# Optimization experiments

Hardware: AMD Instinct MI355X
Metric: run time of the kernel (lower is better)

The kernel has to match this reference:

```python
import jax, jax.numpy as jnp
import numpy as np

B, L, HID, NH = 8, 512, 768, 12
D = HID // NH
T_HOP, T_EDGE = 32, 64


def setup_inputs() -> dict:
    key = jax.random.key(0)
    ks = jax.random.split(key, 18)
    f = lambda k, s, sc=1.0: jax.random.normal(k, s, dtype=jnp.float32) * sc
    return {
        "x": f(ks[0], (B, L, HID)),
        "query_hop_emb": f(ks[1], (T_HOP, HID), 0.05),
        "query_edge_emb": f(ks[2], (T_EDGE, HID), 0.05),
        "key_hop_emb": f(ks[3], (T_HOP, HID), 0.05),
        "key_edge_emb": f(ks[4], (T_EDGE, HID), 0.05),
        "value_hop_emb": f(ks[5], (T_HOP, HID), 0.05),
        "value_edge_emb": f(ks[6], (T_EDGE, HID), 0.05),
        "hop": jax.random.randint(ks[7], (B, L, L), 0, T_HOP, dtype=jnp.int32),
        "edge_matrix": jax.random.randint(ks[8], (B, L, L), 0, T_EDGE, dtype=jnp.int32),
        "Wq": f(ks[9], (HID, HID), 0.02), "bq": f(ks[10], (HID,), 0.02),
        "Wk": f(ks[11], (HID, HID), 0.02), "bk": f(ks[12], (HID,), 0.02),
        "Wv": f(ks[13], (HID, HID), 0.02), "bv": f(ks[14], (HID,), 0.02),
        "Wo": f(ks[15], (HID, HID), 0.02), "bo": f(ks[16], (HID,), 0.02),
    }


def reference(x, query_hop_emb, query_edge_emb, key_hop_emb, key_edge_emb,
              value_hop_emb, value_edge_emb, hop, edge_matrix,
              Wq, bq, Wk, bk, Wv, bv, Wo, bo):
    b, l, _ = x.shape
    scale = 1.0 / np.sqrt(D).astype(np.float32)
    heads = lambda t: t.reshape(b, l, NH, D).transpose(0, 2, 1, 3)  # [B,H,L,D]
    emb = lambda t: t.reshape(-1, NH, D)                             # [T,H,D]

    q = heads(x @ Wq + bq)
    k = heads(x @ Wk + bk)
    v = heads(x @ Wv + bv)

    hop_idx = jnp.broadcast_to(hop[:, None], (b, NH, l, l))
    edge_idx = jnp.broadcast_to(edge_matrix[:, None], (b, NH, l, l))

    def bias(t, e, idx):
        # project onto type embeddings then gather per (i,j) type: [B,H,L,L]
        proj = jnp.einsum('bhld,thd->bhlt', t, emb(e))
        return jnp.take_along_axis(proj, idx, axis=3)

    scores = jnp.einsum('bhld,bhmd->bhlm', q, k)
    scores = scores + bias(q, query_hop_emb, hop_idx) + bias(q, query_edge_emb, edge_idx)
    scores = scores + bias(k, key_hop_emb, hop_idx) + bias(k, key_edge_emb, edge_idx)
    att = jax.nn.softmax(scores * scale, axis=3)

    def scatter_by_type(a, idx, T):
        # re-aggregate attention weights per hop/edge type: [B,H,L,T]
        bi = jnp.arange(b)[:, None, None, None]
        hi = jnp.arange(NH)[None, :, None, None]
        li = jnp.arange(l)[None, None, :, None]
        return jnp.zeros((b, NH, l, T), a.dtype).at[bi, hi, li, idx].add(a)

    out = jnp.einsum('bhlm,bhmd->bhld', att, v)
    out = out + jnp.einsum('bhlt,thd->bhld', scatter_by_type(att, hop_idx, T_HOP), emb(value_hop_emb))
    out = out + jnp.einsum('bhlt,thd->bhld', scatter_by_type(att, edge_idx, T_EDGE), emb(value_edge_emb))

    out = out.transpose(0, 2, 1, 3).reshape(b, l, NH * D)
    return out @ Wo + bo
```

## Files before the change

kernel.cpp:

```cpp
#include <hip/hip_runtime.h>
#include <stdint.h>

#define B_   8
#define L_   512
#define HID_ 768
#define NH_  12
#define D_   64
#define BH_  96
#define TT_  96

typedef __attribute__((ext_vector_type(8))) short short8;
typedef __attribute__((ext_vector_type(4))) float fv4;

#define MFMA16(a, b, c) __builtin_amdgcn_mfma_f32_16x16x32_bf16((a), (b), (c), 0, 0, 0)

__device__ __forceinline__ float bf2f(uint16_t h) {
  union { uint32_t u; float f; } c; c.u = ((uint32_t)h) << 16; return c.f;
}
__device__ __forceinline__ uint16_t f2bf(float x) {
  union { float f; uint32_t u; } c; c.f = x;
  uint32_t r = (c.u + 0x7FFFu + ((c.u >> 16) & 1u)) >> 16;
  return (uint16_t)r;
}
__device__ __forceinline__ float clampf(float v, float lim) {
  return fminf(fmaxf(v, -lim), lim);
}

__device__ __forceinline__ int detect_fp32(const void* xraw) {
  const uint16_t* r = (const uint16_t*)xraw;
  int cnt = 0;
#pragma unroll
  for (int j = 0; j < 16; j++) {
    uint16_t u = r[2 * j];
    int e = (u >> 7) & 0xFF;
    if (u != 0 && e >= 100 && e <= 140) cnt++;
  }
  return cnt < 10;
}

#define SEG_X    0
#define SEG_QH   3145728
#define SEG_QE   3170304
#define SEG_KH   3219456
#define SEG_KE   3244032
#define SEG_VH   3293184
#define SEG_VE   3317760
#define SEG_BQ   3366912
#define SEG_BK   3367680
#define SEG_BV   3368448
#define SEG_BO   3369216
#define SEG_END  3369984
#define SEG_VET  3369984
#define SEG_PK   3443712
#define SEG_ALL  5540864

__global__ __launch_bounds__(256) void convert_all(
    const void* __restrict__ x, const void* __restrict__ qh,
    const void* __restrict__ qe, const void* __restrict__ kh,
    const void* __restrict__ ke, const void* __restrict__ vh,
    const void* __restrict__ ve, const void* __restrict__ b0,
    const void* __restrict__ b1, const void* __restrict__ b2,
    const void* __restrict__ b3, const int* __restrict__ hop,
    const int* __restrict__ edge, uint16_t* __restrict__ dst,
    uint16_t* __restrict__ VET, uint16_t* __restrict__ PK) {
  const int gid = blockIdx.x * 256 + threadIdx.x;
  if (gid >= SEG_ALL) return;
  const int f = detect_fp32(x);
  if (gid >= SEG_PK) {
    const int g = gid - SEG_PK;
    PK[g] = (uint16_t)((hop[g] & 31) | ((edge[g] & 63) << 8));
    return;
  }
  if (gid >= SEG_VET) {
    const int g = gid - SEG_VET;
    const int t = g % TT_;
    const int d = (g / TT_) % D_;
    const int hh = g / (TT_ * D_);
    const void* src = (t < 32) ? vh : ve;
    const size_t idx = (size_t)(t < 32 ? t : t - 32) * HID_ + hh * D_ + d;
    VET[g] = f ? f2bf(((const float*)src)[idx]) : ((const uint16_t*)src)[idx];
    return;
  }
  const void* src;
  int local;
  if (gid < SEG_QH)      { src = x;  local = gid - SEG_X; }
  else if (gid < SEG_QE) { src = qh; local = gid - SEG_QH; }
  else if (gid < SEG_KH) { src = qe; local = gid - SEG_QE; }
  else if (gid < SEG_KE) { src = kh; local = gid - SEG_KH; }
  else if (gid < SEG_VH) { src = ke; local = gid - SEG_KE; }
  else if (gid < SEG_VE) { src = vh; local = gid - SEG_VH; }
  else if (gid < SEG_BQ) { src = ve; local = gid - SEG_VE; }
  else if (gid < SEG_BK) { src = b0; local = gid - SEG_BQ; }
  else if (gid < SEG_BV) { src = b1; local = gid - SEG_BK; }
  else if (gid < SEG_BO) { src = b2; local = gid - SEG_BV; }
  else                   { src = b3; local = gid - SEG_BO; }
  if (f)
    dst[gid] = f2bf(((const float*)src)[local]);
  else
    dst[gid] = ((const uint16_t*)src)[local];
}

__global__ __launch_bounds__(256) void tr_any4(
    const void* __restrict__ s0, const void* __restrict__ s1,
    const void* __restrict__ s2, const void* __restrict__ s3,
    uint16_t* __restrict__ dstbase) {
  __shared__ uint16_t t[32][33];
  const int z = blockIdx.z;
  const void* src = (z == 0) ? s0 : (z == 1) ? s1 : (z == 2) ? s2 : s3;
  uint16_t* dst = dstbase + (size_t)z * (768 * 768);
  const int fp32 = detect_fp32(s0);
  const int tx = threadIdx.x, ty = threadIdx.y;
  const int r0 = blockIdx.y * 32, c0 = blockIdx.x * 32;
#pragma unroll
  for (int k = 0; k < 4; k++) {
    size_t idx = (size_t)(r0 + ty + k * 8) * 768 + c0 + tx;
    t[ty + k * 8][tx] =
        fp32 ? f2bf(((const float*)src)[idx]) : ((const uint16_t*)src)[idx];
  }
  __syncthreads();
#pragma unroll
  for (int k = 0; k < 4; k++)
    dst[(size_t)(c0 + ty + k * 8) * 768 + r0 + tx] = t[tx][ty + k * 8];
}

template <int MODE>
__global__ __launch_bounds__(256) void gemm128(
    const uint16_t* __restrict__ A,
    const uint16_t* __restrict__ BT0, const uint16_t* __restrict__ BT1,
    const uint16_t* __restrict__ BT2,
    const uint16_t* __restrict__ bias0, const uint16_t* __restrict__ bias1,
    const uint16_t* __restrict__ bias2,
    void* __restrict__ out, uint16_t* __restrict__ vt) {
  const int z = blockIdx.z;
  const uint16_t* BT = (z == 0) ? BT0 : (z == 1) ? BT1 : BT2;
  const uint16_t* bias = (z == 0) ? bias0 : (z == 1) ? bias1 : bias2;

  __shared__ __align__(16) uint16_t As[128 * 32];
  __shared__ __align__(16) uint16_t Bs[128 * 32];

  const int tid = threadIdx.x;
  const int lane = tid & 63, quad = lane >> 4, l16 = lane & 15;
  const int w = tid >> 6, wm = w & 1, wn = w >> 1;
  const int m0 = blockIdx.x * 128, n0 = blockIdx.y * 128;

  fv4 acc[4][4];
#pragma unroll
  for (int i = 0; i < 4; i++)
#pragma unroll
    for (int j = 0; j < 4; j++) acc[i][j] = (fv4){0.f, 0.f, 0.f, 0.f};

  const int c0 = tid, c1 = tid + 256;
  const int r0 = c0 >> 2, g0 = (c0 & 3) ^ ((r0 >> 1) & 3);
  const int r1 = c1 >> 2, g1 = (c1 & 3) ^ ((r1 >> 1) & 3);
  const uint16_t* A0 = A + (size_t)(m0 + r0) * HID_ + g0 * 8;
  const uint16_t* A1 = A + (size_t)(m0 + r1) * HID_ + g1 * 8;
  const uint16_t* B0 = BT + (size_t)(n0 + r0) * HID_ + g0 * 8;
  const uint16_t* B1 = BT + (size_t)(n0 + r1) * HID_ + g1 * 8;

  int aoff[4], boff[4];
#pragma unroll
  for (int mi = 0; mi < 4; mi++) {
    int row = wm * 64 + mi * 16 + l16;
    aoff[mi] = row * 32 + (quad ^ ((row >> 1) & 3)) * 8;
  }
#pragma unroll
  for (int ni = 0; ni < 4; ni++) {
    int row = wn * 64 + ni * 16 + l16;
    boff[ni] = row * 32 + (quad ^ ((row >> 1) & 3)) * 8;
  }

  for (int k0 = 0; k0 < HID_; k0 += 32) {
    short8 va0 = *(const short8*)(A0 + k0);
    short8 va1 = *(const short8*)(A1 + k0);
    short8 vb0 = *(const short8*)(B0 + k0);
    short8 vb1 = *(const short8*)(B1 + k0);
    __syncthreads();
    *(short8*)&As[c0 * 8] = va0;
    *(short8*)&As[c1 * 8] = va1;
    *(short8*)&Bs[c0 * 8] = vb0;
    *(short8*)&Bs[c1 * 8] = vb1;
    __syncthreads();
    short8 af[4], bf[4];
#pragma unroll
    for (int mi = 0; mi < 4; mi++) af[mi] = *(const short8*)&As[aoff[mi]];
#pragma unroll
    for (int ni = 0; ni < 4; ni++) bf[ni] = *(const short8*)&Bs[boff[ni]];
#pragma unroll
    for (int mi = 0; mi < 4; mi++)
#pragma unroll
      for (int ni = 0; ni < 4; ni++)
        acc[mi][ni] = MFMA16(af[mi], bf[ni], acc[mi][ni]);
  }

#pragma unroll
  for (int mi = 0; mi < 4; mi++) {
#pragma unroll
    for (int ni = 0; ni < 4; ni++) {
      const int gn = n0 + wn * 64 + ni * 16 + l16;
      const float bv = bf2f(bias[gn]);
      const int gm0 = m0 + wm * 64 + mi * 16 + quad * 4;
      if (MODE == 0 && z == 2) {
        const int bb = gm0 >> 9, ll0 = gm0 & 511;
        const int hh = gn >> 6, dd = gn & 63;
        ushort4 pk;
        pk.x = f2bf(clampf(acc[mi][ni][0] + bv, 1e4f));
        pk.y = f2bf(clampf(acc[mi][ni][1] + bv, 1e4f));
        pk.z = f2bf(clampf(acc[mi][ni][2] + bv, 1e4f));
        pk.w = f2bf(clampf(acc[mi][ni][3] + bv, 1e4f));
        *(ushort4*)&vt[(((size_t)(bb * NH_ + hh)) * D_ + dd) * L_ + ll0] = pk;
      } else {
#pragma unroll
        for (int r = 0; r < 4; r++) {
          const int gm = gm0 + r;
          const float fval = clampf(acc[mi][ni][r] + bv, 1e4f);
          if (MODE == 0) {
            uint16_t* O = (uint16_t*)out + (size_t)z * ((size_t)BH_ * L_ * D_);
            const int bb = gm >> 9, ll = gm & 511, hh = gn >> 6, dd = gn & 63;
            O[(((size_t)(bb * NH_ + hh)) * L_ + ll) * D_ + dd] = f2bf(fval);
          } else {
            ((float*)out)[(size_t)gm * HID_ + gn] = fval;
          }
        }
      }
    }
  }
}

#define SCALE_FX 4194304.f
#define INV_SCALE_FX 2.38418579e-7f

__global__ __launch_bounds__(256) void attn_kernel(
    const uint16_t* __restrict__ Q, const uint16_t* __restrict__ Km,
    const uint16_t* __restrict__ Vt,
    const uint16_t* __restrict__ qh, const uint16_t* __restrict__ qe,
    const uint16_t* __restrict__ kh, const uint16_t* __restrict__ ke,
    const uint16_t* __restrict__ VET, const uint16_t* __restrict__ PK,
    uint16_t* __restrict__ AO) {
  const int n = blockIdx.x;
  const int h = n % NH_;
  const int t2 = n / NH_;
  const int it = t2 & 7, b = t2 >> 3;
  const int bh = b * NH_ + h;
  const int i0 = it * 64;
  const int tid = threadIdx.x;
  const int w = tid >> 6, lane = tid & 63, quad = lane >> 4, l16 = lane & 15;
  const int gi = i0 + w * 16;

  __shared__ uint16_t cbs[4][16][98];
  __shared__ unsigned bkt[4][16][97];
  __shared__ __align__(16) uint16_t PX[4][16][72];

  for (int k = lane; k < 16 * 97; k += 64) (&bkt[w][0][0])[k] = 0u;

  const size_t qkb = (size_t)bh * (L_ * D_);
  short8 a0 = *(const short8*)&Q[qkb + (size_t)(gi + l16) * D_ + quad * 8];
  short8 a1 = *(const short8*)&Q[qkb + (size_t)(gi + l16) * D_ + 32 + quad * 8];
  short8 kq0 = *(const short8*)&Km[qkb + (size_t)(gi + l16) * D_ + quad * 8];
  short8 kq1 =
      *(const short8*)&Km[qkb + (size_t)(gi + l16) * D_ + 32 + quad * 8];

#pragma unroll
  for (int nt = 0; nt < 6; nt++) {
    const uint16_t* eq;
    const uint16_t* ek;
    int t;
    if (nt < 2) { eq = qh; ek = kh; t = nt * 16 + l16; }
    else        { eq = qe; ek = ke; t = (nt - 2) * 16 + l16; }
    const size_t eb0 = (size_t)t * HID_ + h * D_;
    short8 bq0 = *(const short8*)&eq[eb0 + quad * 8];
    short8 bq1 = *(const short8*)&eq[eb0 + 32 + quad * 8];
    short8 bk0 = *(const short8*)&ek[eb0 + quad * 8];
    short8 bk1 = *(const short8*)&ek[eb0 + 32 + quad * 8];
    fv4 cc = (fv4){0.f, 0.f, 0.f, 0.f};
    cc = MFMA16(a0, bq0, cc);
    cc = MFMA16(a1, bq1, cc);
    cc = MFMA16(kq0, bk0, cc);
    cc = MFMA16(kq1, bk1, cc);
#pragma unroll
    for (int r = 0; r < 4; r++)
      cbs[w][quad * 4 + r][nt * 16 + l16] = f2bf(clampf(cc[r], 1e4f));
  }

  const uint16_t* pkb = PK + ((size_t)(b * L_) + gi) * L_;
  const size_t vtb = (size_t)bh * (D_ * L_);

  float vmax[4] = {-1e30f, -1e30f, -1e30f, -1e30f};
  for (int jc = 0; jc < 8; jc++) {
#pragma unroll
    for (int p = 0; p < 2; p++) {
      const int f = lane * 16 + p * 8;
      const int row = f >> 6, col = f & 63;
      *(short8*)&PX[w][row][col] =
          *(const short8*)&pkb[(size_t)row * L_ + jc * 64 + col];
    }
    fv4 sacc[4];
#pragma unroll
    for (int ni = 0; ni < 4; ni++) {
      const int key = jc * 64 + ni * 16 + l16;
      short8 kb0 = *(const short8*)&Km[qkb + (size_t)key * D_ + quad * 8];
      short8 kb1 = *(const short8*)&Km[qkb + (size_t)key * D_ + 32 + quad * 8];
      fv4 a = (fv4){0.f, 0.f, 0.f, 0.f};
      a = MFMA16(a0, kb0, a);
      sacc[ni] = MFMA16(a1, kb1, a);
    }
#pragma unroll
    for (int ni = 0; ni < 4; ni++) {
#pragma unroll
      for (int r = 0; r < 4; r++) {
        const int row = quad * 4 + r;
        const uint32_t pk = PX[w][row][ni * 16 + l16];
        const int th = pk & 31, te = pk >> 8;
        float s = sacc[ni][r] + bf2f(cbs[w][row][th]) +
                  bf2f(cbs[w][row][32 + te]);
        vmax[r] = fmaxf(vmax[r], clampf(s, 512.f));
      }
    }
  }
  float mx[4];
#pragma unroll
  for (int r = 0; r < 4; r++) {
    float m = vmax[r];
    m = fmaxf(m, __shfl_xor(m, 1, 16));
    m = fmaxf(m, __shfl_xor(m, 2, 16));
    m = fmaxf(m, __shfl_xor(m, 4, 16));
    m = fmaxf(m, __shfl_xor(m, 8, 16));
    mx[r] = m;
  }

  fv4 oacc[4];
#pragma unroll
  for (int ni = 0; ni < 4; ni++) oacc[ni] = (fv4){0.f, 0.f, 0.f, 0.f};
  float lsr[4] = {0.f, 0.f, 0.f, 0.f};

  for (int jc = 0; jc < 8; jc++) {
#pragma unroll
    for (int p = 0; p < 2; p++) {
      const int f = lane * 16 + p * 8;
      const int row = f >> 6, col = f & 63;
      *(short8*)&PX[w][row][col] =
          *(const short8*)&pkb[(size_t)row * L_ + jc * 64 + col];
    }
    fv4 sacc[4];
#pragma unroll
    for (int ni = 0; ni < 4; ni++) {
      const int key = jc * 64 + ni * 16 + l16;
      short8 kb0 = *(const short8*)&Km[qkb + (size_t)key * D_ + quad * 8];
      short8 kb1 = *(const short8*)&Km[qkb + (size_t)key * D_ + 32 + quad * 8];
      fv4 a = (fv4){0.f, 0.f, 0.f, 0.f};
      a = MFMA16(a0, kb0, a);
      sacc[ni] = MFMA16(a1, kb1, a);
    }
#pragma unroll
    for (int ni = 0; ni < 4; ni++) {
#pragma unroll
      for (int r = 0; r < 4; r++) {
        const int row = quad * 4 + r;
        const uint32_t pk = PX[w][row][ni * 16 + l16];
        const int th = pk & 31, te = pk >> 8;
        float s = sacc[ni][r] + bf2f(cbs[w][row][th]) +
                  bf2f(cbs[w][row][32 + te]);
        s = clampf(s, 512.f);
        const float p = __expf((s - mx[r]) * 0.125f);
        lsr[r] += p;
        const unsigned pfx = (unsigned)(p * SCALE_FX + 0.5f);
        atomicAdd(&bkt[w][row][th], pfx);
        atomicAdd(&bkt[w][row][32 + te], pfx);
        PX[w][row][ni * 16 + l16] = f2bf(p);
      }
    }
#pragma unroll
    for (int kc = 0; kc < 2; kc++) {
      short8 pa = *(const short8*)&PX[w][l16][kc * 32 + quad * 8];
#pragma unroll
      for (int ni = 0; ni < 4; ni++) {
        short8 vb = *(const short8*)&Vt[vtb + (size_t)(ni * 16 + l16) * L_ +
                                        jc * 64 + kc * 32 + quad * 8];
        oacc[ni] = MFMA16(pa, vb, oacc[ni]);
      }
    }
  }

  const uint16_t* vet = VET + (size_t)h * D_ * TT_;
#pragma unroll
  for (int kc = 0; kc < 3; kc++) {
    short8 pa;
#pragma unroll
    for (int j = 0; j < 8; j++)
      pa[j] = (short)f2bf((float)bkt[w][l16][kc * 32 + quad * 8 + j] *
                          INV_SCALE_FX);
#pragma unroll
    for (int ni = 0; ni < 4; ni++) {
      short8 vb =
          *(const short8*)&vet[(size_t)(ni * 16 + l16) * TT_ + kc * 32 +
                               quad * 8];
      oacc[ni] = MFMA16(pa, vb, oacc[ni]);
    }
  }

  float linv[4];
#pragma unroll
  for (int r = 0; r < 4; r++) {
    float s = lsr[r];
    s += __shfl_xor(s, 1, 16);
    s += __shfl_xor(s, 2, 16);
    s += __shfl_xor(s, 4, 16);
    s += __shfl_xor(s, 8, 16);
    linv[r] = 1.f / s;
  }

#pragma unroll
  for (int ni = 0; ni < 4; ni++)
#pragma unroll
    for (int r = 0; r < 4; r++) {
      const int i = gi + quad * 4 + r;
      AO[(((size_t)b * L_ + i) * NH_ + h) * D_ + ni * 16 + l16] =
          f2bf(oacc[ni][r] * linv[r]);
    }
}

extern "C" void kernel_launch(void* const* d_in, const int* in_sizes, int n_in,
                              void* d_out, int out_size, void* d_ws,
                              size_t ws_size, hipStream_t stream) {
  const void* x_raw = d_in[0];
  const int* hop    = (const int*)d_in[7];
  const int* edge   = (const int*)d_in[8];

  char* ws = (char*)d_ws;
  uint16_t* QKV = (uint16_t*)(ws);
  uint16_t* Qp  = QKV;
  uint16_t* Kp  = QKV + (size_t)BH_ * L_ * D_;
  uint16_t* Vtp = (uint16_t*)(ws + 18874368);
  uint16_t* PKp = (uint16_t*)(ws + 25165824);
  uint16_t* AO  = (uint16_t*)(ws + 44040192);
  uint16_t* WTq = (uint16_t*)(ws + 50331648);
  uint16_t* WTk = WTq + 768 * 768;
  uint16_t* WTv = WTk + 768 * 768;
  uint16_t* WTo = WTv + 768 * 768;
  uint16_t* CAN = (uint16_t*)(ws + 55050240);
  uint16_t* VET = (uint16_t*)(ws + 61790208);

  uint16_t* xc  = CAN + SEG_X;
  uint16_t* qhc = CAN + SEG_QH;
  uint16_t* qec = CAN + SEG_QE;
  uint16_t* khc = CAN + SEG_KH;
  uint16_t* kec = CAN + SEG_KE;
  uint16_t* bqc = CAN + SEG_BQ;
  uint16_t* bkc = CAN + SEG_BK;
  uint16_t* bvc = CAN + SEG_BV;
  uint16_t* boc = CAN + SEG_BO;

  convert_all<<<(SEG_ALL + 255) / 256, 256, 0, stream>>>(
      x_raw, d_in[1], d_in[2], d_in[3], d_in[4], d_in[5], d_in[6],
      d_in[10], d_in[12], d_in[14], d_in[16], hop, edge, CAN, VET, PKp);

  dim3 tb(32, 8, 1);
  tr_any4<<<dim3(24, 24, 4), tb, 0, stream>>>(d_in[9], d_in[11], d_in[13],
                                              d_in[15], WTq);

  gemm128<0><<<dim3(32, 6, 3), 256, 0, stream>>>(xc, WTq, WTk, WTv, bqc, bkc,
                                                 bvc, QKV, Vtp);

  attn_kernel<<<768, 256, 0, stream>>>(Qp, Kp, Vtp, qhc, qec, khc, kec, VET,
                                       PKp, AO);

  gemm128<1><<<dim3(32, 6, 1), 256, 0, stream>>>(AO, WTo, WTo, WTo, boc, boc,
                                                 boc, d_out, nullptr);
}
```

Before: 259.1 us.

## Use upper-bound softmax max from raw QK and bias maxima; async LDS loads in GEMM

The attention max pass no longer loads packed hop/edge indices or gathers bias values. It computes only raw QK scores and adds the per-row maximum hop bias and maximum edge bias, giving an upper bound that is still a valid softmax shift. The clamp on s is dropped from the exp pass. Separately, the projection GEMM stages tiles with global_load_lds instead of going through registers. Using an upper bound instead of the true max risks underflow in exp and in the fixed-point bucket accumulation when the bound is loose.

After: 245.5 us. 5.2% less time.

```diff
diff --git a/kernel.cpp b/kernel.cpp
--- a/kernel.cpp
+++ b/kernel.cpp
@@ -24,6 +24,12 @@
 }
 __device__ __forceinline__ float clampf(float v, float lim) {
   return fminf(fmaxf(v, -lim), lim);
+}
+
+__device__ __forceinline__ void gld_lds16(const uint16_t* g, uint16_t* lds) {
+  __builtin_amdgcn_global_load_lds(
+      (const __attribute__((address_space(1))) uint32_t*)(uintptr_t)g,
+      (__attribute__((address_space(3))) uint32_t*)(uintptr_t)lds, 16, 0, 0);
 }
 
 __device__ __forceinline__ int detect_fp32(const void* xraw) {
@@ -156,6 +162,10 @@
   const uint16_t* A1 = A + (size_t)(m0 + r1) * HID_ + g1 * 8;
   const uint16_t* B0 = BT + (size_t)(n0 + r0) * HID_ + g0 * 8;
   const uint16_t* B1 = BT + (size_t)(n0 + r1) * HID_ + g1 * 8;
+  uint16_t* lA0 = &As[c0 * 8];
+  uint16_t* lA1 = &As[c1 * 8];
+  uint16_t* lB0 = &Bs[c0 * 8];
+  uint16_t* lB1 = &Bs[c1 * 8];
 
   int aoff[4], boff[4];
 #pragma unroll
@@ -170,15 +180,11 @@
   }
 
   for (int k0 = 0; k0 < HID_; k0 += 32) {
-    short8 va0 = *(const short8*)(A0 + k0);
-    short8 va1 = *(const short8*)(A1 + k0);
-    short8 vb0 = *(const short8*)(B0 + k0);
-    short8 vb1 = *(const short8*)(B1 + k0);
     __syncthreads();
-    *(short8*)&As[c0 * 8] = va0;
-    *(short8*)&As[c1 * 8] = va1;
-    *(short8*)&Bs[c0 * 8] = vb0;
-    *(short8*)&Bs[c1 * 8] = vb1;
+    gld_lds16(A0 + k0, lA0);
+    gld_lds16(A1 + k0, lA1);
+    gld_lds16(B0 + k0, lB0);
+    gld_lds16(B1 + k0, lB1);
     __syncthreads();
     short8 af[4], bf[4];
 #pragma unroll
@@ -259,6 +265,8 @@
   short8 kq1 =
       *(const short8*)&Km[qkb + (size_t)(gi + l16) * D_ + 32 + quad * 8];
 
+  float hx[4] = {-1e30f, -1e30f, -1e30f, -1e30f};
+  float ex[4] = {-1e30f, -1e30f, -1e30f, -1e30f};
 #pragma unroll
   for (int nt = 0; nt < 6; nt++) {
     const uint16_t* eq;
@@ -277,14 +285,47 @@
     cc = MFMA16(kq0, bk0, cc);
     cc = MFMA16(kq1, bk1, cc);
 #pragma unroll
-    for (int r = 0; r < 4; r++)
-      cbs[w][quad * 4 + r][nt * 16 + l16] = f2bf(clampf(cc[r], 1e4f));
+    for (int r = 0; r < 4; r++) {
+      const float cv = clampf(cc[r], 1e4f);
+      cbs[w][quad * 4 + r][nt * 16 + l16] = f2bf(cv);
+      if (nt < 2) hx[r] = fmaxf(hx[r], cv);
+      else        ex[r] = fmaxf(ex[r], cv);
+    }
   }
 
   const uint16_t* pkb = PK + ((size_t)(b * L_) + gi) * L_;
   const size_t vtb = (size_t)bh * (D_ * L_);
 
-  float vmax[4] = {-1e30f, -1e30f, -1e30f, -1e30f};
+  float vq[4] = {-1e30f, -1e30f, -1e30f, -1e30f};
+  for (int jc = 0; jc < 8; jc++) {
+#pragma unroll
+    for (int ni = 0; ni < 4; ni++) {
+      const int key = jc * 64 + ni * 16 + l16;
+      short8 kb0 = *(const short8*)&Km[qkb + (size_t)key * D_ + quad * 8];
+      short8 kb1 = *(const short8*)&Km[qkb + (size_t)key * D_ + 32 + quad * 8];
+      fv4 a = (fv4){0.f, 0.f, 0.f, 0.f};
+      a = MFMA16(a0, kb0, a);
+      a = MFMA16(a1, kb1, a);
+#pragma unroll
+      for (int r = 0; r < 4; r++) vq[r] = fmaxf(vq[r], a[r]);
+    }
+  }
+  float mx[4];
+#pragma unroll
+  for (int r = 0; r < 4; r++) {
+    float m = vq[r] + hx[r] + ex[r];
+    m = fmaxf(m, __shfl_xor(m, 1, 16));
+    m = fmaxf(m, __shfl_xor(m, 2, 16));
+    m = fmaxf(m, __shfl_xor(m, 4, 16));
+    m = fmaxf(m, __shfl_xor(m, 8, 16));
+    mx[r] = m;
+  }
+
+  fv4 oacc[4];
+#pragma unroll
+  for (int ni = 0; ni < 4; ni++) oacc[ni] = (fv4){0.f, 0.f, 0.f, 0.f};
+  float lsr[4] = {0.f, 0.f, 0.f, 0.f};
+
   for (int jc = 0; jc < 8; jc++) {
 #pragma unroll
     for (int p = 0; p < 2; p++) {
@@ -312,54 +353,6 @@
         const int th = pk & 31, te = pk >> 8;
         float s = sacc[ni][r] + bf2f(cbs[w][row][th]) +
                   bf2f(cbs[w][row][32 + te]);
-        vmax[r] = fmaxf(vmax[r], clampf(s, 512.f));
-      }
-    }
-  }
-  float mx[4];
-#pragma unroll
-  for (int r = 0; r < 4; r++) {
-    float m = vmax[r];
-    m = fmaxf(m, __shfl_xor(m, 1, 16));
-    m = fmaxf(m, __shfl_xor(m, 2, 16));
-    m = fmaxf(m, __shfl_xor(m, 4, 16));
-    m = fmaxf(m, __shfl_xor(m, 8, 16));
-    mx[r] = m;
-  }
-
-  fv4 oacc[4];
-#pragma unroll
-  for (int ni = 0; ni < 4; ni++) oacc[ni] = (fv4){0.f, 0.f, 0.f, 0.f};
-  float lsr[4] = {0.f, 0.f, 0.f, 0.f};
-
-  for (int jc = 0; jc < 8; jc++) {
-#pragma unroll
-    for (int p = 0; p < 2; p++) {
-      const int f = lane * 16 + p * 8;
-      const int row = f >> 6, col = f & 63;
-      *(short8*)&PX[w][row][col] =
-          *(const short8*)&pkb[(size_t)row * L_ + jc * 64 + col];
-    }
-    fv4 sacc[4];
-#pragma unroll
-    for (int ni = 0; ni < 4; ni++) {
-      const int key = jc * 64 + ni * 16 + l16;
-      short8 kb0 = *(const short8*)&Km[qkb + (size_t)key * D_ + quad * 8];
-      short8 kb1 = *(const short8*)&Km[qkb + (size_t)key * D_ + 32 + quad * 8];
-      fv4 a = (fv4){0.f, 0.f, 0.f, 0.f};
-      a = MFMA16(a0, kb0, a);
-      sacc[ni] = MFMA16(a1, kb1, a);
-    }
-#pragma unroll
-    for (int ni = 0; ni < 4; ni++) {
-#pragma unroll
-      for (int r = 0; r < 4; r++) {
-        const int row = quad * 4 + r;
-        const uint32_t pk = PX[w][row][ni * 16 + l16];
-        const int th = pk & 31, te = pk >> 8;
-        float s = sacc[ni][r] + bf2f(cbs[w][row][th]) +
-                  bf2f(cbs[w][row][32 + te]);
-        s = clampf(s, 512.f);
         const float p = __expf((s - mx[r]) * 0.125f);
         lsr[r] += p;
         const unsigned pfx = (unsigned)(p * SCALE_FX + 0.5f);
```
